# Kernel optimization log

Hardware: AMD Instinct MI355X
Metric: run time of the kernel (lower is better)

Reference implementation:

```python
import jax, jax.numpy as jnp
import numpy as np

jax.config.update("jax_enable_x64", True)  # hash uses int64 multiply-xor like torch .long()

NUM_LEVELS = 16
LEVEL_DIM = 2
PER_LEVEL_SCALE = 2
BASE_RES = 16
LOG2_HASHMAP = 19
PS1 = 19349663  # second spatial hash prime (ps[0] == 1)
N_POINTS = 524288


def _isprime(n):
    for p in range(2, int(n ** 0.5) + 1):
        if n % p == 0:
            return False
    return True


N_ENTRIES = 2 ** LOG2_HASHMAP
while not _isprime(N_ENTRIES):
    N_ENTRIES += 1  # -> 524309

SCALES = []
OFFSETS = [0]
START_HASH = NUM_LEVELS  # module uses -1 sentinel; NUM_LEVELS == 'no hashing yet'
for i in range(NUM_LEVELS):
    res = int(BASE_RES * PER_LEVEL_SCALE ** i)
    SCALES.append(res)
    n = (res + 1) ** 2
    if n > N_ENTRIES:
        if START_HASH == NUM_LEVELS:
            START_HASH = i
        n = N_ENTRIES
    OFFSETS.append(OFFSETS[-1] + n)
TABLE_SIZE = OFFSETS[-1]  # 5594552

CORNERS = jnp.array([[0.0, 0.0], [0.0, 1.0], [1.0, 0.0], [1.0, 1.0]], dtype=jnp.float32)  # [4,2]
SCALES_F = jnp.array(SCALES, dtype=jnp.float32)          # [L]
SCALES_I = jnp.array(SCALES, dtype=jnp.int64)            # [L]
LEVEL_OFF = jnp.array(OFFSETS[:-1], dtype=jnp.int64)     # [L] base offset per level


def setup_inputs() -> dict:
    key = jax.random.key(0)
    k1, k2 = jax.random.split(key)
    x = jax.random.uniform(k1, (N_POINTS, 2), dtype=jnp.float32)  # coords in [0,1)
    data = (jax.random.uniform(k2, (TABLE_SIZE, LEVEL_DIM), dtype=jnp.float32) * 2.0 - 1.0) * 1e-4
    return {"x": x, "data": data}


def reference(x, data):
    L, F = NUM_LEVELS, LEVEL_DIM
    float_x = x[None] * SCALES_F[:, None, None]                                  # [L,N,2]
    int_x = (float_x[:, :, None, :] + CORNERS[None, None]).astype(jnp.int64)     # [L,N,4,2]
    offset_x = float_x - int_x[:, :, 0].astype(float_x.dtype)                    # [L,N,2] frac part
    ix0, ix1 = int_x[..., 0], int_x[..., 1]
    # dense-grid index for low levels, spatial hash for high levels
    grid_ind = ix0 * (SCALES_I + 1)[:, None, None] + ix1                         # [L,N,4]
    hash_ind = (ix0 ^ (ix1 * PS1)) % N_ENTRIES                                   # [L,N,4]
    is_grid = (jnp.arange(L) < START_HASH)[:, None, None]
    ind = jnp.where(is_grid, grid_ind, hash_ind) + LEVEL_OFF[:, None, None]      # [L,N,4]
    val = data[ind]                                                              # [L,N,4,F]
    # bilinear corner weights: clamp(1 - c + (2c-1)*frac) per axis, product over xy
    w = jnp.clip(1.0 - CORNERS[None, None] + (2.0 * CORNERS[None, None] - 1.0) * offset_x[:, :, None], 0.0, 1.0)
    w = w[..., 0] * w[..., 1]                                                    # [L,N,4]
    out = jnp.einsum('lnc,lncf->lnf', w, val)                                    # [L,N,F]
    return out.transpose(1, 0, 2).reshape(-1, L * F)                             # [N, L*F]
```

## Files before the change

kernel.cpp:

```cpp
#include <hip/hip_runtime.h>


static constexpr int  kPoints    = 524288;
static constexpr int  kLevels    = 16;
static constexpr int  kStartHash = 6;
static constexpr unsigned kPs1     = 19349663u;
static constexpr unsigned kEntries = 524309u;
static constexpr unsigned kR32     = 352277u;

typedef float v4f __attribute__((ext_vector_type(4)));

__device__ __forceinline__ void nt_store4(float4* p, const float4 v) {
    v4f t; t.x = v.x; t.y = v.y; t.z = v.z; t.w = v.w;
    __builtin_nontemporal_store(t, (v4f*)p);
}

__constant__ unsigned c_level_off[kLevels] = {
    0u, 289u, 1378u, 5603u, 22244u, 88293u, 351462u,
    875771u, 1400080u, 1924389u, 2448698u, 2973007u,
    3497316u, 4021625u, 4545934u, 5070243u
};

struct Corners {
    float    w00, w01, w10, w11;
    unsigned i00, i01, i10, i11;
};

__device__ __forceinline__ Corners prep_level(const float2 p, const int l)
{
    const int   scale_i = 16 << l;
    const float scale_f = (float)scale_i;

    const float fx = p.x * scale_f;
    const float fy = p.y * scale_f;

    const unsigned ix0 = (unsigned)(int)fx;
    const unsigned iy0 = (unsigned)(int)fy;
    const unsigned ix1 = (unsigned)(int)(fx + 1.0f);
    const unsigned iy1 = (unsigned)(int)(fy + 1.0f);

    const float ox = fx - (float)ix0;
    const float oy = fy - (float)iy0;

    const float wx1 = fminf(fmaxf(ox, 0.0f), 1.0f);
    const float wx0 = fminf(fmaxf(1.0f - ox, 0.0f), 1.0f);
    const float wy1 = fminf(fmaxf(oy, 0.0f), 1.0f);
    const float wy0 = fminf(fmaxf(1.0f - oy, 0.0f), 1.0f);

    unsigned i00, i01, i10, i11;
    if (l < kStartHash) {
        const unsigned stride = (unsigned)(scale_i + 1);
        i00 = ix0 * stride + iy0;
        i01 = ix0 * stride + iy1;
        i10 = ix1 * stride + iy0;
        i11 = ix1 * stride + iy1;
    } else {
        const unsigned long long hy0 = (unsigned long long)iy0 * kPs1;
        const unsigned long long hy1 = (unsigned long long)iy1 * kPs1;
        const unsigned lo0 = (unsigned)hy0, hi0 = (unsigned)(hy0 >> 32);
        const unsigned lo1 = (unsigned)hy1, hi1 = (unsigned)(hy1 >> 32);
        const unsigned a0 = (hi0 * kR32) % kEntries;
        const unsigned a1 = (hi1 * kR32) % kEntries;
        i00 = a0 + ((lo0 ^ ix0) % kEntries); if (i00 >= kEntries) i00 -= kEntries;
        i01 = a1 + ((lo1 ^ ix0) % kEntries); if (i01 >= kEntries) i01 -= kEntries;
        i10 = a0 + ((lo0 ^ ix1) % kEntries); if (i10 >= kEntries) i10 -= kEntries;
        i11 = a1 + ((lo1 ^ ix1) % kEntries); if (i11 >= kEntries) i11 -= kEntries;
    }

    Corners c;
    const unsigned base = c_level_off[l];
    c.i00 = base + i00; c.i01 = base + i01;
    c.i10 = base + i10; c.i11 = base + i11;
    c.w00 = wx0 * wy0;  c.w01 = wx0 * wy1;
    c.w10 = wx1 * wy0;  c.w11 = wx1 * wy1;
    return c;
}

__device__ __forceinline__ void load_pair(
    const float2* __restrict__ tbl, const unsigned ia, const unsigned ib,
    float2& va, float2& vb)
{
    if (ib == ia + 1u && !(ia & 1u)) {
        const v4f q = *reinterpret_cast<const v4f*>(&tbl[ia]);
        va = make_float2(q.x, q.y);
        vb = make_float2(q.z, q.w);
    } else {
        va = tbl[ia];
        vb = tbl[ib];
    }
}

__global__ __launch_bounds__(256) void level_pass(
    const float2* __restrict__ x,
    const float2* __restrict__ tbl,
    float2* __restrict__ ws)
{
    const int b    = blockIdx.x;
    const int xcd  = b & 7;
    const int slot = b >> 3;

    int level, pblk;
    if (slot < 2048) {
        level = 6 + xcd;
        pblk  = slot;
    } else if (slot < 2304) {
        level = 14;
        pblk  = xcd * 256 + (slot - 2048);
    } else if (slot < 2560) {
        level = 15;
        pblk  = xcd * 256 + (slot - 2304);
    } else {
        const int d = xcd * 1536 + (slot - 2560);
        level = d >> 11;
        pblk  = d & 2047;
    }

    const int n = (pblk << 8) | threadIdx.x;
    const float2 p = x[n];
    const Corners c = prep_level(p, level);

    float2 v00, v01, v10, v11;
    if (level < kStartHash) {
        load_pair(tbl, c.i00, c.i01, v00, v01);
        load_pair(tbl, c.i10, c.i11, v10, v11);
    } else {
        load_pair(tbl, c.i00, c.i10, v00, v10);
        load_pair(tbl, c.i01, c.i11, v01, v11);
    }

    const float2 r = make_float2(
        c.w00 * v00.x + c.w01 * v01.x + c.w10 * v10.x + c.w11 * v11.x,
        c.w00 * v00.y + c.w01 * v01.y + c.w10 * v10.y + c.w11 * v11.y);

    ws[((size_t)pblk << 12) + (level << 8) + threadIdx.x] = r;
}

static constexpr int kT2S = 66;

__global__ __launch_bounds__(256) void transpose_out(
    const float2* __restrict__ ws,
    float4* __restrict__ out)
{
    __shared__ float2 lds[kLevels][kT2S];

    const int t = threadIdx.x;
    const int b = blockIdx.x;
    const int chunk = b >> 2;
    const int coff  = (b & 3) << 6;
    const float2* __restrict__ base = ws + ((size_t)chunk << 12) + coff;

#pragma unroll
    for (int k = 0; k < 4; ++k) {
        const int e = (k << 8) + t;
        const int l = e >> 6;
        const int cc = e & 63;
        lds[l][cc] = base[(l << 8) + cc];
    }

    __syncthreads();

    float4* o = out + ((size_t)b << 9);
#pragma unroll
    for (int k = 0; k < 2; ++k) {
        const int g  = (k << 8) + t;
        const int nl = g >> 3;
        const int i  = g & 7;
        const float2 a  = lds[2 * i][nl];
        const float2 bb = lds[2 * i + 1][nl];
        nt_store4(&o[g], make_float4(a.x, a.y, bb.x, bb.y));
    }
}

__global__ __launch_bounds__(256) void hashgrid_fwd(
    const float2* __restrict__ x,
    const float2* __restrict__ tbl,
    float4* __restrict__ out)
{
    const int n = blockIdx.x * blockDim.x + threadIdx.x;
    if (n >= kPoints) return;
    const float2 p = x[n];
    float acc[2 * kLevels];
#pragma unroll
    for (int l = 0; l < kLevels; ++l) {
        const Corners c = prep_level(p, l);
        const float2 v00 = tbl[c.i00], v01 = tbl[c.i01];
        const float2 v10 = tbl[c.i10], v11 = tbl[c.i11];
        acc[2 * l + 0] = c.w00 * v00.x + c.w01 * v01.x + c.w10 * v10.x + c.w11 * v11.x;
        acc[2 * l + 1] = c.w00 * v00.y + c.w01 * v01.y + c.w10 * v10.y + c.w11 * v11.y;
    }
    float4* o = out + (size_t)n * 8;
#pragma unroll
    for (int i = 0; i < 8; ++i)
        o[i] = make_float4(acc[4 * i + 0], acc[4 * i + 1],
                           acc[4 * i + 2], acc[4 * i + 3]);
}

extern "C" void kernel_launch(void* const* d_in, const int* in_sizes, int n_in,
                              void* d_out, int out_size, void* d_ws, size_t ws_size,
                              hipStream_t stream) {
    const float2* x   = (const float2*)d_in[0];
    const float2* tbl = (const float2*)d_in[1];

    const size_t ws_needed = (size_t)kLevels * kPoints * sizeof(float2);
    if (ws_size >= ws_needed) {
        float2* ws = (float2*)d_ws;
        level_pass<<<kLevels * (kPoints / 256), 256, 0, stream>>>(x, tbl, ws);
        transpose_out<<<kPoints / 64, 256, 0, stream>>>(ws, (float4*)d_out);
    } else {
        hashgrid_fwd<<<kPoints / 256, 256, 0, stream>>>(x, tbl, (float4*)d_out);
    }
}
```

Before: 211.8 us.

## Batch levels 14-15 and dense levels per block; relax paired-load alignment

Blocks for the two largest hashed levels now compute both levels per point, and blocks for the six dense-grid levels compute all six, so the grid shrinks from 16x to 10x the point blocks. This reuses the point load and index setup and cuts block count. The paired 16-byte load now also fires for unaligned and reverse-ordered adjacent indices, using memcpy to allow unaligned vector loads. The fallback kernel also uses the paired gather path. The cost is longer per-thread work and a less even balance across XCDs.

```diff
diff --git a/kernel.cpp b/kernel.cpp
--- a/kernel.cpp
+++ b/kernel.cpp
@@ -80,14 +80,34 @@
     const float2* __restrict__ tbl, const unsigned ia, const unsigned ib,
     float2& va, float2& vb)
 {
-    if (ib == ia + 1u && !(ia & 1u)) {
-        const v4f q = *reinterpret_cast<const v4f*>(&tbl[ia]);
+    if (ib == ia + 1u) {
+        v4f q; __builtin_memcpy(&q, &tbl[ia], 16);
         va = make_float2(q.x, q.y);
         vb = make_float2(q.z, q.w);
+    } else if (ia == ib + 1u) {
+        v4f q; __builtin_memcpy(&q, &tbl[ib], 16);
+        vb = make_float2(q.x, q.y);
+        va = make_float2(q.z, q.w);
     } else {
         va = tbl[ia];
         vb = tbl[ib];
     }
+}
+
+__device__ __forceinline__ float2 gather_level(
+    const float2* __restrict__ tbl, const Corners& c, const bool hashed)
+{
+    float2 v00, v01, v10, v11;
+    if (!hashed) {
+        load_pair(tbl, c.i00, c.i01, v00, v01);
+        load_pair(tbl, c.i10, c.i11, v10, v11);
+    } else {
+        load_pair(tbl, c.i00, c.i10, v00, v10);
+        load_pair(tbl, c.i01, c.i11, v01, v11);
+    }
+    return make_float2(
+        c.w00 * v00.x + c.w01 * v01.x + c.w10 * v10.x + c.w11 * v11.x,
+        c.w00 * v00.y + c.w01 * v01.y + c.w10 * v10.y + c.w11 * v11.y);
 }
 
 __global__ __launch_bounds__(256) void level_pass(
@@ -99,40 +119,34 @@
     const int xcd  = b & 7;
     const int slot = b >> 3;
 
-    int level, pblk;
     if (slot < 2048) {
-        level = 6 + xcd;
-        pblk  = slot;
+        const int level = 6 + xcd;
+        const int pblk  = slot;
+        const int n = (pblk << 8) | threadIdx.x;
+        const float2 p = x[n];
+        const float2 r = gather_level(tbl, prep_level(p, level), true);
+        ws[((size_t)pblk << 12) + (level << 8) + threadIdx.x] = r;
     } else if (slot < 2304) {
-        level = 14;
-        pblk  = xcd * 256 + (slot - 2048);
-    } else if (slot < 2560) {
-        level = 15;
-        pblk  = xcd * 256 + (slot - 2304);
-    } else {
-        const int d = xcd * 1536 + (slot - 2560);
-        level = d >> 11;
-        pblk  = d & 2047;
-    }
-
-    const int n = (pblk << 8) | threadIdx.x;
-    const float2 p = x[n];
-    const Corners c = prep_level(p, level);
-
-    float2 v00, v01, v10, v11;
-    if (level < kStartHash) {
-        load_pair(tbl, c.i00, c.i01, v00, v01);
-        load_pair(tbl, c.i10, c.i11, v10, v11);
-    } else {
-        load_pair(tbl, c.i00, c.i10, v00, v10);
-        load_pair(tbl, c.i01, c.i11, v01, v11);
-    }
-
-    const float2 r = make_float2(
-        c.w00 * v00.x + c.w01 * v01.x + c.w10 * v10.x + c.w11 * v11.x,
-        c.w00 * v00.y + c.w01 * v01.y + c.w10 * v10.y + c.w11 * v11.y);
-
-    ws[((size_t)pblk << 12) + (level << 8) + threadIdx.x] = r;
+        const int pblk = xcd * 256 + (slot - 2048);
+        const int n = (pblk << 8) | threadIdx.x;
+        const float2 p = x[n];
+        const size_t wb = ((size_t)pblk << 12) + threadIdx.x;
+#pragma unroll
+        for (int level = 14; level <= 15; ++level) {
+            const float2 r = gather_level(tbl, prep_level(p, level), true);
+            ws[wb + (level << 8)] = r;
+        }
+    } else {
+        const int pblk = xcd * 256 + (slot - 2304);
+        const int n = (pblk << 8) | threadIdx.x;
+        const float2 p = x[n];
+        const size_t wb = ((size_t)pblk << 12) + threadIdx.x;
+#pragma unroll
+        for (int level = 0; level < kStartHash; ++level) {
+            const float2 r = gather_level(tbl, prep_level(p, level), false);
+            ws[wb + (level << 8)] = r;
+        }
+    }
 }
 
 static constexpr int kT2S = 66;
@@ -182,11 +196,9 @@
     float acc[2 * kLevels];
 #pragma unroll
     for (int l = 0; l < kLevels; ++l) {
-        const Corners c = prep_level(p, l);
-        const float2 v00 = tbl[c.i00], v01 = tbl[c.i01];
-        const float2 v10 = tbl[c.i10], v11 = tbl[c.i11];
-        acc[2 * l + 0] = c.w00 * v00.x + c.w01 * v01.x + c.w10 * v10.x + c.w11 * v11.x;
-        acc[2 * l + 1] = c.w00 * v00.y + c.w01 * v01.y + c.w10 * v10.y + c.w11 * v11.y;
+        const float2 r = gather_level(tbl, prep_level(p, l), l >= kStartHash);
+        acc[2 * l + 0] = r.x;
+        acc[2 * l + 1] = r.y;
     }
     float4* o = out + (size_t)n * 8;
 #pragma unroll
@@ -204,7 +216,7 @@
     const size_t ws_needed = (size_t)kLevels * kPoints * sizeof(float2);
     if (ws_size >= ws_needed) {
         float2* ws = (float2*)d_ws;
-        level_pass<<<kLevels * (kPoints / 256), 256, 0, stream>>>(x, tbl, ws);
+        level_pass<<<2560 * 8, 256, 0, stream>>>(x, tbl, ws);
         transpose_out<<<kPoints / 64, 256, 0, stream>>>(ws, (float4*)d_out);
     } else {
         hashgrid_fwd<<<kPoints / 256, 256, 0, stream>>>(x, tbl, (float4*)d_out);
```

Measured after the change: 202.2 us. 1.05x faster.
